# Kernel tuning notes

Measured on AMD Instinct MI355X. Metric: run time of the kernel, lower is better.

Reference implementation:

```python
import jax, jax.numpy as jnp
import numpy as np

B, S, E, H = 4, 2048, 2048, 16
D = E // H  # head_dim = 128
MAX_LEN = 2048


def _make_freqs():
    # standard RoPE frequencies: theta = 10000^{-2i/D}
    inv_freq = 1.0 / (10000.0 ** (np.arange(0, D, 2, dtype=np.float32) / D))  # [D/2]
    t = np.arange(MAX_LEN, dtype=np.float32)
    ang = np.outer(t, inv_freq)  # [max_len, D/2]
    cos = ang.reshape(1, MAX_LEN, 1, D // 2)
    return jnp.asarray(np.cos(cos)), jnp.asarray(np.sin(cos))


def setup_inputs() -> dict:
    key = jax.random.key(0)
    ks = jax.random.split(key, 10)
    sc = 1.0 / np.sqrt(E)
    freqs_cos, freqs_sin = _make_freqs()
    return {
        "x": jax.random.normal(ks[0], (B, S, E), dtype=jnp.float32),
        "freqs_cos": freqs_cos,
        "freqs_sin": freqs_sin,
        "wq": jax.random.normal(ks[1], (E, E), dtype=jnp.float32) * sc,
        "bq": jax.random.normal(ks[2], (E,), dtype=jnp.float32) * 0.01,
        "wk": jax.random.normal(ks[3], (E, E), dtype=jnp.float32) * sc,
        "bk": jax.random.normal(ks[4], (E,), dtype=jnp.float32) * 0.01,
        "wv": jax.random.normal(ks[5], (E, E), dtype=jnp.float32) * sc,
        "bv": jax.random.normal(ks[6], (E,), dtype=jnp.float32) * 0.01,
        "wo": jax.random.normal(ks[7], (E, E), dtype=jnp.float32) * sc,
        "bo": jax.random.normal(ks[8], (E,), dtype=jnp.float32) * 0.01,
    }


def _rope(t, cos, sin):
    # t: [B, S, H, D]; complex multiply on interleaved (even, odd) pairs
    tr = t.reshape(*t.shape[:-1], -1, 2)  # [B,S,H,D/2,2]
    xr, xi = tr[..., 0], tr[..., 1]
    rr = xr * cos - xi * sin
    ri = xr * sin + xi * cos
    return jnp.stack([rr, ri], axis=-1).reshape(t.shape)


def reference(x, freqs_cos, freqs_sin, wq, bq, wk, bk, wv, bv, wo, bo):
    b, s, _ = x.shape
    q = (x @ wq.T + bq).reshape(b, s, H, D)
    k = (x @ wk.T + bk).reshape(b, s, H, D)
    v = (x @ wv.T + bv).reshape(b, s, H, D)
    cos, sin = freqs_cos[:, :s], freqs_sin[:, :s]
    q = _rope(q, cos, sin)
    k = _rope(k, cos, sin)
    # FAITHFUL to source: q,k,v stay [B,S,H,D], so matmul contracts over D
    # producing per-position head-head scores [B,S,H,H] (no transpose to BHSD).
    qk = jnp.einsum("bshd,bsgd->bshg", q, k) / jnp.sqrt(jnp.float32(D))
    att = jax.nn.softmax(qk, axis=-1)
    att_out = jnp.einsum("bshg,bsgd->bshd", att, v)  # [B,S,H,D]
    # torch: transpose(1,2).contiguous().view(B,S,-1) -> h-major flatten
    att_out = jnp.transpose(att_out, (0, 2, 1, 3)).reshape(b, s, -1)
    return att_out @ wo.T + bo
```

## Files before the change

kernel.cpp:

```cpp
#include <hip/hip_runtime.h>
#include <stdint.h>

typedef unsigned short u16t;
typedef __attribute__((ext_vector_type(8))) short frag8;
typedef __attribute__((ext_vector_type(4))) float facc4;

#define S_LEN 2048
#define E_DIM 2048
#define M_TOT 8192

__device__ __forceinline__ u16t f2bf(float f) {
    union { float f; uint32_t u; } c; c.f = f;
    return (u16t)((c.u + 0x7fffu + ((c.u >> 16) & 1u)) >> 16);
}
__device__ __forceinline__ float bfu2f(uint32_t u) {
    union { uint32_t u; float f; } c; c.u = u << 16;
    return c.f;
}

__global__ __launch_bounds__(256) void cvt_kernel(const float* __restrict__ src,
                                                  u16t* __restrict__ dst, int n4) {
    int i = blockIdx.x * 256 + threadIdx.x;
    if (i >= n4) return;
    float4 v = ((const float4*)src)[i];
    ushort4 o;
    o.x = f2bf(v.x); o.y = f2bf(v.y); o.z = f2bf(v.z); o.w = f2bf(v.w);
    ((ushort4*)dst)[i] = o;
}

__device__ __forceinline__ void gldl16(const u16t* g, u16t* l) {
    __builtin_amdgcn_global_load_lds(
        (__attribute__((address_space(1))) void*)(g),
        (__attribute__((address_space(3))) void*)(l), 16, 0, 0);
}

__device__ __forceinline__ void gemm_core(const u16t* __restrict__ A,
                                          const u16t* __restrict__ Bw,
                                          u16t* As, u16t* Bs,
                                          facc4 acc[4][4]) {
    const int t    = threadIdx.x;
    const int lane = t & 63;
    const int wid  = t >> 6;
    const int m16  = lane & 15;
    const int quad = lane >> 4;
    const int wm   = (wid & 1) * 64;
    const int wn   = (wid >> 1) * 64;
    const size_t bm0 = (size_t)blockIdx.y * 128;
    const size_t bn0 = (size_t)blockIdx.x * 128;

#pragma unroll
    for (int i = 0; i < 4; ++i)
#pragma unroll
        for (int j = 0; j < 4; ++j) acc[i][j] = facc4{0.f, 0.f, 0.f, 0.f};

    const u16t* Ab = A + bm0 * E_DIM;
    const u16t* Bb = Bw + bn0 * E_DIM;

    const int e0 = wid * 512;
    const int e1 = 2048 + wid * 512;
    const int le0 = e0 + lane * 8, le1 = e1 + lane * 8;
    const int r0 = le0 >> 5, c0 = le0 & 31;
    const int r1 = le1 >> 5, c1 = le1 & 31;

    for (int k0 = 0; k0 < E_DIM; k0 += 32) {
        __syncthreads();
        gldl16(Ab + (size_t)r0 * E_DIM + k0 + c0, As + e0);
        gldl16(Ab + (size_t)r1 * E_DIM + k0 + c1, As + e1);
        gldl16(Bb + (size_t)r0 * E_DIM + k0 + c0, Bs + e0);
        gldl16(Bb + (size_t)r1 * E_DIM + k0 + c1, Bs + e1);
        __syncthreads();

        frag8 av[4], bv[4];
#pragma unroll
        for (int i = 0; i < 4; ++i)
            av[i] = *(const frag8*)(As + (wm + i * 16 + m16) * 32 + quad * 8);
#pragma unroll
        for (int j = 0; j < 4; ++j)
            bv[j] = *(const frag8*)(Bs + (wn + j * 16 + m16) * 32 + quad * 8);
#pragma unroll
        for (int i = 0; i < 4; ++i)
#pragma unroll
            for (int j = 0; j < 4; ++j)
                acc[i][j] = __builtin_amdgcn_mfma_f32_16x16x32_bf16(
                    av[i], bv[j], acc[i][j], 0, 0, 0);
    }
}

struct QkvArgs {
    const u16t* w[3];
    const float* bias[3];
    u16t* out[3];
};

__global__ __launch_bounds__(256, 2)
void qkv_gemm(const u16t* __restrict__ xb, QkvArgs args,
              const float* __restrict__ fcos, const float* __restrict__ fsin) {
    __shared__ u16t As[128 * 32];
    __shared__ u16t Bs[128 * 32];
    facc4 acc[4][4];
    const int z = blockIdx.z;
    gemm_core(xb, args.w[z], As, Bs, acc);

    const int t    = threadIdx.x;
    const int lane = t & 63;
    const int m16  = lane & 15;
    const int quad = lane >> 4;
    const int wid  = t >> 6;
    const int wm   = (wid & 1) * 64;
    const int wn   = (wid >> 1) * 64;
    const int bm0  = blockIdx.y * 128;
    const int bn0  = blockIdx.x * 128;
    const bool rope = (z < 2);
    u16t* out = args.out[z];
    const float* bias = args.bias[z];

#pragma unroll
    for (int i = 0; i < 4; ++i) {
#pragma unroll
        for (int j = 0; j < 4; ++j) {
            const int n = bn0 + wn + j * 16 + m16;
            const float bn_ = bias[n];
#pragma unroll
            for (int r = 0; r < 4; ++r) {
                const int m = bm0 + wm + i * 16 + quad * 4 + r;
                float v = acc[i][j][r] + bn_;
                const float part = __shfl_xor(v, 1, 64);
                if (rope) {
                    const int s = m & (S_LEN - 1);
                    const int p = (n & 127) >> 1;
                    const float cs = fcos[s * 64 + p];
                    const float sn = fsin[s * 64 + p];
                    v = (n & 1) ? (part * sn + v * cs) : (v * cs - part * sn);
                }
                out[(size_t)m * E_DIM + n] = f2bf(v);
            }
        }
    }
}

__global__ __launch_bounds__(256, 2)
void out_gemm(const u16t* __restrict__ sh, const u16t* __restrict__ wob,
              const float* __restrict__ bo, float* __restrict__ out) {
    __shared__ u16t As[128 * 32];
    __shared__ u16t Bs[128 * 32];
    facc4 acc[4][4];
    gemm_core(sh, wob, As, Bs, acc);

    const int t    = threadIdx.x;
    const int lane = t & 63;
    const int m16  = lane & 15;
    const int quad = lane >> 4;
    const int wid  = t >> 6;
    const int wm   = (wid & 1) * 64;
    const int wn   = (wid >> 1) * 64;
    const int bm0  = blockIdx.y * 128;
    const int bn0  = blockIdx.x * 128;

#pragma unroll
    for (int i = 0; i < 4; ++i) {
#pragma unroll
        for (int j = 0; j < 4; ++j) {
            const int n = bn0 + wn + j * 16 + m16;
            const float bn_ = bo[n];
#pragma unroll
            for (int r = 0; r < 4; ++r) {
                const int m = bm0 + wm + i * 16 + quad * 4 + r;
                out[(size_t)m * E_DIM + n] = acc[i][j][r] + bn_;
            }
        }
    }
}

__global__ __launch_bounds__(256)
void attn_kernel(const u16t* __restrict__ qb, const u16t* __restrict__ kb,
                 const u16t* __restrict__ vb, u16t* __restrict__ sh) {
    __shared__ float Q[16][132];
    __shared__ float Kt[16][132];
    __shared__ float V[16][132];
    __shared__ float P[16][17];

    const int tk = blockIdx.x;
    const int b  = tk >> 11;
    const int s  = tk & (S_LEN - 1);
    const int t  = threadIdx.x;
    const size_t row = (size_t)tk * E_DIM;

    const int rr = t >> 4;
    const int cc = (t & 15) * 8;

    {
        uint4 pq = *(const uint4*)(qb + row + t * 8);
        uint4 pk = *(const uint4*)(kb + row + t * 8);
        uint4 pv = *(const uint4*)(vb + row + t * 8);
        float* qd = &Q[rr][cc];  float* kd = &Kt[rr][cc];  float* vd = &V[rr][cc];
        qd[0] = bfu2f(pq.x & 0xffff); qd[1] = bfu2f(pq.x >> 16);
        qd[2] = bfu2f(pq.y & 0xffff); qd[3] = bfu2f(pq.y >> 16);
        qd[4] = bfu2f(pq.z & 0xffff); qd[5] = bfu2f(pq.z >> 16);
        qd[6] = bfu2f(pq.w & 0xffff); qd[7] = bfu2f(pq.w >> 16);
        kd[0] = bfu2f(pk.x & 0xffff); kd[1] = bfu2f(pk.x >> 16);
        kd[2] = bfu2f(pk.y & 0xffff); kd[3] = bfu2f(pk.y >> 16);
        kd[4] = bfu2f(pk.z & 0xffff); kd[5] = bfu2f(pk.z >> 16);
        kd[6] = bfu2f(pk.w & 0xffff); kd[7] = bfu2f(pk.w >> 16);
        vd[0] = bfu2f(pv.x & 0xffff); vd[1] = bfu2f(pv.x >> 16);
        vd[2] = bfu2f(pv.y & 0xffff); vd[3] = bfu2f(pv.y >> 16);
        vd[4] = bfu2f(pv.z & 0xffff); vd[5] = bfu2f(pv.z >> 16);
        vd[6] = bfu2f(pv.w & 0xffff); vd[7] = bfu2f(pv.w >> 16);
    }
    __syncthreads();

    const int g = t & 15;
    float sc = 0.f;
#pragma unroll 16
    for (int d = 0; d < 128; ++d) sc = fmaf(Q[rr][d], Kt[g][d], sc);
    sc *= 0.08838834764831845f;

    float mx = sc;
#pragma unroll
    for (int msk = 1; msk < 16; msk <<= 1) mx = fmaxf(mx, __shfl_xor(mx, msk, 64));
    float ex = __expf(sc - mx);
    float sm = ex;
#pragma unroll
    for (int msk = 1; msk < 16; msk <<= 1) sm += __shfl_xor(sm, msk, 64);
    P[rr][g] = ex / sm;
    __syncthreads();

    float o[8];
#pragma unroll
    for (int i = 0; i < 8; ++i) o[i] = 0.f;
#pragma unroll
    for (int gg = 0; gg < 16; ++gg) {
        const float p = P[rr][gg];
#pragma unroll
        for (int i = 0; i < 8; ++i) o[i] = fmaf(p, V[gg][cc + i], o[i]);
    }
    union { u16t us[8]; uint4 v; } pko;
#pragma unroll
    for (int i = 0; i < 8; ++i) pko.us[i] = f2bf(o[i]);
    const size_t dst = ((size_t)b << 22)
                     + (size_t)(rr * 128 + (s >> 4)) * E_DIM
                     + (size_t)((s & 15) * 128 + cc);
    *(uint4*)(sh + dst) = pko.v;
}

extern "C" void kernel_launch(void* const* d_in, const int* in_sizes, int n_in,
                              void* d_out, int out_size, void* d_ws, size_t ws_size,
                              hipStream_t stream) {
    const float* x    = (const float*)d_in[0];
    const float* fcos = (const float*)d_in[1];
    const float* fsin = (const float*)d_in[2];
    const float* wq   = (const float*)d_in[3];
    const float* bq   = (const float*)d_in[4];
    const float* wk   = (const float*)d_in[5];
    const float* bk   = (const float*)d_in[6];
    const float* wv   = (const float*)d_in[7];
    const float* bv   = (const float*)d_in[8];
    const float* wo   = (const float*)d_in[9];
    const float* bo   = (const float*)d_in[10];
    float* out = (float*)d_out;

    char* ws = (char*)d_ws;
    u16t* xb  = (u16t*)(ws);
    u16t* qb  = (u16t*)(ws + 33554432ull);
    u16t* kb  = (u16t*)(ws + 67108864ull);
    u16t* vb  = (u16t*)(ws + 100663296ull);
    u16t* wqb = (u16t*)(ws + 134217728ull);
    u16t* wkb = (u16t*)(ws + 142606336ull);
    u16t* wvb = (u16t*)(ws + 150994944ull);
    u16t* wob = (u16t*)(ws + 159383552ull);

    cvt_kernel<<<16384, 256, 0, stream>>>(x, xb, 4194304);
    cvt_kernel<<<4096, 256, 0, stream>>>(wq, wqb, 1048576);
    cvt_kernel<<<4096, 256, 0, stream>>>(wk, wkb, 1048576);
    cvt_kernel<<<4096, 256, 0, stream>>>(wv, wvb, 1048576);
    cvt_kernel<<<4096, 256, 0, stream>>>(wo, wob, 1048576);

    QkvArgs qa;
    qa.w[0] = wqb; qa.w[1] = wkb; qa.w[2] = wvb;
    qa.bias[0] = bq; qa.bias[1] = bk; qa.bias[2] = bv;
    qa.out[0] = qb; qa.out[1] = kb; qa.out[2] = vb;
    qkv_gemm<<<dim3(16, 64, 3), 256, 0, stream>>>(xb, qa, fcos, fsin);

    attn_kernel<<<8192, 256, 0, stream>>>(qb, kb, vb, xb);

    out_gemm<<<dim3(16, 64), 256, 0, stream>>>(xb, wob, bo, out);
}
```

Measured before the change: 584.6 us.

## Use MFMA for per-token head attention and double the GEMM K-step

```diff
diff --git a/kernel.cpp b/kernel.cpp
--- a/kernel.cpp
+++ b/kernel.cpp
@@ -7,15 +7,10 @@
 
 #define S_LEN 2048
 #define E_DIM 2048
-#define M_TOT 8192
 
 __device__ __forceinline__ u16t f2bf(float f) {
     union { float f; uint32_t u; } c; c.f = f;
     return (u16t)((c.u + 0x7fffu + ((c.u >> 16) & 1u)) >> 16);
-}
-__device__ __forceinline__ float bfu2f(uint32_t u) {
-    union { uint32_t u; float f; } c; c.u = u << 16;
-    return c.f;
 }
 
 __global__ __launch_bounds__(256) void cvt_kernel(const float* __restrict__ src,
@@ -36,7 +31,8 @@
 
 __device__ __forceinline__ void gemm_core(const u16t* __restrict__ A,
                                           const u16t* __restrict__ Bw,
-                                          u16t* As, u16t* Bs,
+                                          u16t* As0, u16t* As1,
+                                          u16t* Bs0, u16t* Bs1,
                                           facc4 acc[4][4]) {
     const int t    = threadIdx.x;
     const int lane = t & 63;
@@ -61,28 +57,39 @@
     const int le0 = e0 + lane * 8, le1 = e1 + lane * 8;
     const int r0 = le0 >> 5, c0 = le0 & 31;
     const int r1 = le1 >> 5, c1 = le1 & 31;
-
-    for (int k0 = 0; k0 < E_DIM; k0 += 32) {
+    const size_t ga0 = (size_t)r0 * E_DIM + c0;
+    const size_t ga1 = (size_t)r1 * E_DIM + c1;
+
+    for (int k0 = 0; k0 < E_DIM; k0 += 64) {
         __syncthreads();
-        gldl16(Ab + (size_t)r0 * E_DIM + k0 + c0, As + e0);
-        gldl16(Ab + (size_t)r1 * E_DIM + k0 + c1, As + e1);
-        gldl16(Bb + (size_t)r0 * E_DIM + k0 + c0, Bs + e0);
-        gldl16(Bb + (size_t)r1 * E_DIM + k0 + c1, Bs + e1);
+        gldl16(Ab + ga0 + k0,      As0 + e0);
+        gldl16(Ab + ga1 + k0,      As0 + e1);
+        gldl16(Ab + ga0 + k0 + 32, As1 + e0);
+        gldl16(Ab + ga1 + k0 + 32, As1 + e1);
+        gldl16(Bb + ga0 + k0,      Bs0 + e0);
+        gldl16(Bb + ga1 + k0,      Bs0 + e1);
+        gldl16(Bb + ga0 + k0 + 32, Bs1 + e0);
+        gldl16(Bb + ga1 + k0 + 32, Bs1 + e1);
         __syncthreads();
 
-        frag8 av[4], bv[4];
-#pragma unroll
-        for (int i = 0; i < 4; ++i)
-            av[i] = *(const frag8*)(As + (wm + i * 16 + m16) * 32 + quad * 8);
-#pragma unroll
-        for (int j = 0; j < 4; ++j)
-            bv[j] = *(const frag8*)(Bs + (wn + j * 16 + m16) * 32 + quad * 8);
-#pragma unroll
-        for (int i = 0; i < 4; ++i)
+#pragma unroll
+        for (int h = 0; h < 2; ++h) {
+            const u16t* Ah = h ? As1 : As0;
+            const u16t* Bh = h ? Bs1 : Bs0;
+            frag8 av[4], bv[4];
+#pragma unroll
+            for (int i = 0; i < 4; ++i)
+                av[i] = *(const frag8*)(Ah + (wm + i * 16 + m16) * 32 + quad * 8);
 #pragma unroll
             for (int j = 0; j < 4; ++j)
-                acc[i][j] = __builtin_amdgcn_mfma_f32_16x16x32_bf16(
-                    av[i], bv[j], acc[i][j], 0, 0, 0);
+                bv[j] = *(const frag8*)(Bh + (wn + j * 16 + m16) * 32 + quad * 8);
+#pragma unroll
+            for (int i = 0; i < 4; ++i)
+#pragma unroll
+                for (int j = 0; j < 4; ++j)
+                    acc[i][j] = __builtin_amdgcn_mfma_f32_16x16x32_bf16(
+                        av[i], bv[j], acc[i][j], 0, 0, 0);
+        }
     }
 }
 
@@ -95,11 +102,11 @@
 __global__ __launch_bounds__(256, 2)
 void qkv_gemm(const u16t* __restrict__ xb, QkvArgs args,
               const float* __restrict__ fcos, const float* __restrict__ fsin) {
-    __shared__ u16t As[128 * 32];
-    __shared__ u16t Bs[128 * 32];
+    __shared__ u16t As0[128 * 32], As1[128 * 32];
+    __shared__ u16t Bs0[128 * 32], Bs1[128 * 32];
     facc4 acc[4][4];
     const int z = blockIdx.z;
-    gemm_core(xb, args.w[z], As, Bs, acc);
+    gemm_core(xb, args.w[z], As0, As1, Bs0, Bs1, acc);
 
     const int t    = threadIdx.x;
     const int lane = t & 63;
@@ -141,10 +148,10 @@
 __global__ __launch_bounds__(256, 2)
 void out_gemm(const u16t* __restrict__ sh, const u16t* __restrict__ wob,
               const float* __restrict__ bo, float* __restrict__ out) {
-    __shared__ u16t As[128 * 32];
-    __shared__ u16t Bs[128 * 32];
+    __shared__ u16t As0[128 * 32], As1[128 * 32];
+    __shared__ u16t Bs0[128 * 32], Bs1[128 * 32];
     facc4 acc[4][4];
-    gemm_core(sh, wob, As, Bs, acc);
+    gemm_core(sh, wob, As0, As1, Bs0, Bs1, acc);
 
     const int t    = threadIdx.x;
     const int lane = t & 63;
@@ -174,72 +181,88 @@
 __global__ __launch_bounds__(256)
 void attn_kernel(const u16t* __restrict__ qb, const u16t* __restrict__ kb,
                  const u16t* __restrict__ vb, u16t* __restrict__ sh) {
-    __shared__ float Q[16][132];
-    __shared__ float Kt[16][132];
-    __shared__ float V[16][132];
-    __shared__ float P[16][17];
-
-    const int tk = blockIdx.x;
-    const int b  = tk >> 11;
-    const int s  = tk & (S_LEN - 1);
-    const int t  = threadIdx.x;
+    __shared__ u16t Vs[4][16 * 136];
+    __shared__ u16t Pt[4][16 * 32];
+
+    const int t    = threadIdx.x;
+    const int wid  = t >> 6;
+    const int lane = t & 63;
+    const int m16  = lane & 15;
+    const int quad = lane >> 4;
+    const int tk   = blockIdx.x * 4 + wid;
+    const int b    = tk >> 11;
+    const int s    = tk & (S_LEN - 1);
     const size_t row = (size_t)tk * E_DIM;
 
-    const int rr = t >> 4;
-    const int cc = (t & 15) * 8;
-
-    {
-        uint4 pq = *(const uint4*)(qb + row + t * 8);
-        uint4 pk = *(const uint4*)(kb + row + t * 8);
-        uint4 pv = *(const uint4*)(vb + row + t * 8);
-        float* qd = &Q[rr][cc];  float* kd = &Kt[rr][cc];  float* vd = &V[rr][cc];
-        qd[0] = bfu2f(pq.x & 0xffff); qd[1] = bfu2f(pq.x >> 16);
-        qd[2] = bfu2f(pq.y & 0xffff); qd[3] = bfu2f(pq.y >> 16);
-        qd[4] = bfu2f(pq.z & 0xffff); qd[5] = bfu2f(pq.z >> 16);
-        qd[6] = bfu2f(pq.w & 0xffff); qd[7] = bfu2f(pq.w >> 16);
-        kd[0] = bfu2f(pk.x & 0xffff); kd[1] = bfu2f(pk.x >> 16);
-        kd[2] = bfu2f(pk.y & 0xffff); kd[3] = bfu2f(pk.y >> 16);
-        kd[4] = bfu2f(pk.z & 0xffff); kd[5] = bfu2f(pk.z >> 16);
-        kd[6] = bfu2f(pk.w & 0xffff); kd[7] = bfu2f(pk.w >> 16);
-        vd[0] = bfu2f(pv.x & 0xffff); vd[1] = bfu2f(pv.x >> 16);
-        vd[2] = bfu2f(pv.y & 0xffff); vd[3] = bfu2f(pv.y >> 16);
-        vd[4] = bfu2f(pv.z & 0xffff); vd[5] = bfu2f(pv.z >> 16);
-        vd[6] = bfu2f(pv.w & 0xffff); vd[7] = bfu2f(pv.w >> 16);
-    }
+    frag8 aq[4], ak[4];
+    const u16t* qrow = qb + row + m16 * 128 + quad * 8;
+    const u16t* krow = kb + row + m16 * 128 + quad * 8;
+#pragma unroll
+    for (int ks = 0; ks < 4; ++ks) {
+        aq[ks] = *(const frag8*)(qrow + ks * 32);
+        ak[ks] = *(const frag8*)(krow + ks * 32);
+    }
+
+    u16t* vs = Vs[wid];
+#pragma unroll
+    for (int c = 0; c < 4; ++c) {
+        const int e  = c * 512 + lane * 8;
+        const int vr = e >> 7, vc = e & 127;
+        *(uint4*)(vs + vr * 136 + vc) = *(const uint4*)(vb + row + e);
+    }
+
+    facc4 sacc = facc4{0.f, 0.f, 0.f, 0.f};
+#pragma unroll
+    for (int ks = 0; ks < 4; ++ks)
+        sacc = __builtin_amdgcn_mfma_f32_16x16x32_bf16(aq[ks], ak[ks], sacc, 0, 0, 0);
+
+    float p[4], mx[4], sm[4];
+#pragma unroll
+    for (int r = 0; r < 4; ++r) { p[r] = sacc[r] * 0.08838834764831845f; mx[r] = p[r]; }
+#pragma unroll
+    for (int msk = 1; msk < 16; msk <<= 1)
+#pragma unroll
+        for (int r = 0; r < 4; ++r) mx[r] = fmaxf(mx[r], __shfl_xor(mx[r], msk, 64));
+#pragma unroll
+    for (int r = 0; r < 4; ++r) { p[r] = __expf(p[r] - mx[r]); sm[r] = p[r]; }
+#pragma unroll
+    for (int msk = 1; msk < 16; msk <<= 1)
+#pragma unroll
+        for (int r = 0; r < 4; ++r) sm[r] += __shfl_xor(sm[r], msk, 64);
+
+    u16t* pt = Pt[wid];
+#pragma unroll
+    for (int r = 0; r < 4; ++r)
+        pt[(quad * 4 + r) * 32 + m16] = f2bf(p[r] / sm[r]);
+    *(uint2*)(pt + m16 * 32 + 16 + quad * 4) = uint2{0u, 0u};
+
     __syncthreads();
 
-    const int g = t & 15;
-    float sc = 0.f;
-#pragma unroll 16
-    for (int d = 0; d < 128; ++d) sc = fmaf(Q[rr][d], Kt[g][d], sc);
-    sc *= 0.08838834764831845f;
-
-    float mx = sc;
-#pragma unroll
-    for (int msk = 1; msk < 16; msk <<= 1) mx = fmaxf(mx, __shfl_xor(mx, msk, 64));
-    float ex = __expf(sc - mx);
-    float sm = ex;
-#pragma unroll
-    for (int msk = 1; msk < 16; msk <<= 1) sm += __shfl_xor(sm, msk, 64);
-    P[rr][g] = ex / sm;
-    __syncthreads();
-
-    float o[8];
-#pragma unroll
-    for (int i = 0; i < 8; ++i) o[i] = 0.f;
-#pragma unroll
-    for (int gg = 0; gg < 16; ++gg) {
-        const float p = P[rr][gg];
-#pragma unroll
-        for (int i = 0; i < 8; ++i) o[i] = fmaf(p, V[gg][cc + i], o[i]);
-    }
-    union { u16t us[8]; uint4 v; } pko;
-#pragma unroll
-    for (int i = 0; i < 8; ++i) pko.us[i] = f2bf(o[i]);
-    const size_t dst = ((size_t)b << 22)
-                     + (size_t)(rr * 128 + (s >> 4)) * E_DIM
-                     + (size_t)((s & 15) * 128 + cc);
-    *(uint4*)(sh + dst) = pko.v;
+    const frag8 aP = *(const frag8*)(pt + m16 * 32 + quad * 8);
+
+    facc4 oacc[8];
+#pragma unroll
+    for (int d = 0; d < 8; ++d) oacc[d] = facc4{0.f, 0.f, 0.f, 0.f};
+#pragma unroll
+    for (int dblk = 0; dblk < 8; ++dblk) {
+        union { u16t u[8]; frag8 f; } bb;
+#pragma unroll
+        for (int j = 0; j < 8; ++j)
+            bb.u[j] = vs[((quad * 8 + j) & 15) * 136 + dblk * 16 + m16];
+        oacc[dblk] = __builtin_amdgcn_mfma_f32_16x16x32_bf16(aP, bb.f, oacc[dblk], 0, 0, 0);
+    }
+
+    const size_t base = ((size_t)b << 22) + (size_t)(s >> 4) * E_DIM
+                      + (size_t)((s & 15) * 128);
+#pragma unroll
+    for (int dblk = 0; dblk < 8; ++dblk) {
+        const int d = dblk * 16 + m16;
+#pragma unroll
+        for (int r = 0; r < 4; ++r) {
+            const int h = quad * 4 + r;
+            sh[base + ((size_t)h << 18) + d] = f2bf(oacc[dblk][r]);
+        }
+    }
 }
 
 extern "C" void kernel_launch(void* const* d_in, const int* in_sizes, int n_in,
@@ -280,7 +303,7 @@
     qa.out[0] = qb; qa.out[1] = kb; qa.out[2] = vb;
     qkv_gemm<<<dim3(16, 64, 3), 256, 0, stream>>>(xb, qa, fcos, fsin);
 
-    attn_kernel<<<8192, 256, 0, stream>>>(qb, kb, vb, xb);
+    attn_kernel<<<2048, 256, 0, stream>>>(qb, kb, vb, xb);
 
     out_gemm<<<dim3(16, 64), 256, 0, stream>>>(xb, wob, bo, out);
 }
```

After: 520.0 us. 1.12x faster.
